# Kernel tuning notes

Measured on AMD Instinct MI355X. Metric: run time of the kernel, lower is better.

Reference implementation:

```python
import jax, jax.numpy as jnp
import numpy as np

B, C, T = 128, 9, 2048
R = T // 4            # reduced_timesteps after two MaxPool1d(2)
N = B * R             # total graph nodes
E_SINGLE = 8192       # edges per sample graph (avg degree 16 over R nodes)
HID = 128
OUT = 12


def setup_inputs():
    key = jax.random.key(0)
    ks = jax.random.split(key, 14)
    x = jax.random.normal(ks[0], (B, C, T), jnp.float32)
    # per-sample graph, replicated with offset i*R per batch element (as in forward)
    single = jax.random.randint(ks[1], (2, E_SINGLE), 0, R)
    offsets = (jnp.arange(B) * R)[None, :, None]
    edge_index = (single[:, None, :] + offsets).reshape(2, -1)  # [2, B*E_SINGLE]

    def lin(k, fan_in, shape):
        return jax.random.normal(k, shape, jnp.float32) / np.sqrt(fan_in)

    return {
        "x": x,
        "edge_index": edge_index,
        "conv1_w": lin(ks[2], C * 5, (16, C, 5)),
        "conv1_b": jnp.zeros((16,), jnp.float32),
        "conv2_w": lin(ks[3], 16 * 5, (32, 16, 5)),
        "conv2_b": jnp.zeros((32,), jnp.float32),
        "gcn1_w": lin(ks[4], 32, (32, HID)),
        "gcn1_b": jnp.zeros((HID,), jnp.float32),
        "gcn2_w": lin(ks[5], HID, (HID, HID)),
        "gcn2_b": jnp.zeros((HID,), jnp.float32),
        "fc_w": lin(ks[6], HID, (HID, OUT)),
        "fc_b": jnp.zeros((OUT,), jnp.float32),
    }


def _gcn_conv(h, edge_index, w, b, n):
    # PyG GCNConv: linear -> add self-loops -> sym-normalized sum aggregation -> + bias
    h = h @ w
    loops = jnp.arange(n)
    row = jnp.concatenate([edge_index[0], loops])  # source
    col = jnp.concatenate([edge_index[1], loops])  # target (aggregation)
    deg = jax.ops.segment_sum(jnp.ones(col.shape, h.dtype), col, num_segments=n)
    dis = jnp.where(deg > 0, jax.lax.rsqrt(jnp.maximum(deg, 1e-12)), 0.0)
    norm = dis[row] * dis[col]                      # [E+N]
    out = jax.ops.segment_sum(norm[:, None] * h[row], col, num_segments=n)
    return out + b


def _temporal_conv(x, w1, b1, w2, b2):
    dn = ("NCH", "OIH", "NCH")
    h = jax.lax.conv_general_dilated(x, w1, (1,), [(2, 2)], dimension_numbers=dn)
    h = jax.nn.relu(h + b1[None, :, None])
    h = jax.lax.reduce_window(h, -jnp.inf, jax.lax.max, (1, 1, 2), (1, 1, 2), "VALID")
    h = jax.lax.conv_general_dilated(h, w2, (1,), [(2, 2)], dimension_numbers=dn)
    h = jax.nn.relu(h + b2[None, :, None])
    h = jax.lax.reduce_window(h, -jnp.inf, jax.lax.max, (1, 1, 2), (1, 1, 2), "VALID")
    return h  # [B, 32, R]


def reference(x, edge_index, conv1_w, conv1_b, conv2_w, conv2_b,
              gcn1_w, gcn1_b, gcn2_w, gcn2_b, fc_w, fc_b):
    h = _temporal_conv(x, conv1_w, conv1_b, conv2_w, conv2_b)   # [B, 32, R]
    nodes = h.transpose(0, 2, 1).reshape(B * R, 32)             # [N, 32]
    g = jax.nn.relu(_gcn_conv(nodes, edge_index, gcn1_w, gcn1_b, N))
    g = jax.nn.relu(_gcn_conv(g, edge_index, gcn2_w, gcn2_b, N))
    g = g.reshape(B, R, HID).mean(axis=1)                       # [B, HID]
    return g @ fc_w + fc_b                                      # [B, OUT]
```

## Files before the change

### kernel.cpp

```cpp
#include <hip/hip_runtime.h>
#include <hip/hip_bf16.h>

#define BB   128
#define CIN  9
#define TT   2048
#define RR   512
#define NN   (BB*RR)
#define HID  128
#define NOUT 12

typedef __attribute__((ext_vector_type(8))) short short8;
typedef __attribute__((ext_vector_type(4))) float f32x4;

static __device__ inline unsigned short f2bf(float f) {
    unsigned int u = __float_as_uint(f);
    unsigned int r = (u + 0x7fffu + ((u >> 16) & 1u)) >> 16;
    return (unsigned short)r;
}
static __device__ inline float bf2f(unsigned short u) {
    return __uint_as_float(((unsigned int)u) << 16);
}

__global__ __launch_bounds__(512) void k_convs(const float* __restrict__ x,
        const float* __restrict__ w1, const float* __restrict__ b1,
        const float* __restrict__ w2, const float* __restrict__ b2,
        unsigned short* __restrict__ nodes16,
        const int* __restrict__ ei, int E, int es,
        int* __restrict__ rptr, float* __restrict__ dis, int* __restrict__ adj,
        const float* __restrict__ g2w, unsigned short* __restrict__ w2t) {
    __shared__ float sx[CIN][268];
    __shared__ float s1[16][132];
    __shared__ int lcnt[512];
    __shared__ int sp[512];
    __shared__ int lcur[512];
    int tid = threadIdx.x;

    if (blockIdx.x == 0) {
        int t = tid;
        lcnt[t] = 0;
        __syncthreads();
        for (int i = t; i < es; i += 512) atomicAdd(&lcnt[ei[E + i]], 1);
        __syncthreads();
        int c = lcnt[t];
        sp[t] = c;
        __syncthreads();
        for (int off = 1; off < 512; off <<= 1) {
            int v = sp[t];
            int add = (t >= off) ? sp[t - off] : 0;
            __syncthreads();
            sp[t] = v + add;
            __syncthreads();
        }
        int excl = sp[t] - c;
        rptr[t] = excl;
        if (t == 511) rptr[512] = es;
        dis[t] = rsqrtf((float)c + 1.0f);
        lcur[t] = excl;
        __syncthreads();
        for (int i = t; i < es; i += 512) {
            int row = ei[i], col = ei[E + i];
            int pos = atomicAdd(&lcur[col], 1);
            adj[pos] = row;
        }
        for (int idx = t; idx < 128 * 128; idx += 512) {
            int c2 = idx >> 7, f = idx & 127;
            w2t[f * 128 + c2] = f2bf(g2w[idx]);
        }
        return;
    }

    int cb = blockIdx.x - 1;
    int b  = cb >> 3;
    int r0 = (cb & 7) * 64;
    int wv   = __builtin_amdgcn_readfirstlane(tid >> 6);
    int lane = tid & 63;

    for (int idx = tid; idx < CIN * 268; idx += 512) {
        int c = idx / 268, j = idx - c * 268;
        int g = 4 * r0 - 6 + j;
        float v = 0.f;
        if (g >= 0 && g < TT) v = x[(b * CIN + c) * TT + g];
        sx[c][j] = v;
    }
    __syncthreads();

    {
        int c1a = wv * 2, c1b = wv * 2 + 1;
        float biasA = b1[c1a], biasB = b1[c1b];
        for (int pp = lane; pp < 132; pp += 64) {
            int p = 2 * r0 - 2 + pp;
            float valA = 0.f, valB = 0.f;
            if (p >= 0 && p < 1024) {
                float a0A = biasA, a1A = biasA, a0B = biasB, a1B = biasB;
#pragma unroll
                for (int c = 0; c < CIN; ++c) {
                    const float2* px = (const float2*)&sx[c][2 * pp];
                    float2 q0 = px[0], q1 = px[1], q2 = px[2];
                    {
                        const float* wp = &w1[(c1a * CIN + c) * 5];
                        float k0 = wp[0], k1 = wp[1], k2 = wp[2], k3 = wp[3], k4 = wp[4];
                        a0A += q0.x*k0 + q0.y*k1 + q1.x*k2 + q1.y*k3 + q2.x*k4;
                        a1A += q0.y*k0 + q1.x*k1 + q1.y*k2 + q2.x*k3 + q2.y*k4;
                    }
                    {
                        const float* wp = &w1[(c1b * CIN + c) * 5];
                        float k0 = wp[0], k1 = wp[1], k2 = wp[2], k3 = wp[3], k4 = wp[4];
                        a0B += q0.x*k0 + q0.y*k1 + q1.x*k2 + q1.y*k3 + q2.x*k4;
                        a1B += q0.y*k0 + q1.x*k1 + q1.y*k2 + q2.x*k3 + q2.y*k4;
                    }
                }
                valA = fmaxf(fmaxf(a0A, a1A), 0.f);
                valB = fmaxf(fmaxf(a0B, a1B), 0.f);
            }
            s1[c1a][pp] = valA;
            s1[c1b][pp] = valB;
        }
    }
    __syncthreads();

    int rl = lane;
    float acc0[4], acc1[4];
#pragma unroll
    for (int o = 0; o < 4; ++o) {
        float bv = b2[wv * 4 + o];
        acc0[o] = bv; acc1[o] = bv;
    }
#pragma unroll
    for (int c = 0; c < 16; ++c) {
        const float2* ps = (const float2*)&s1[c][2 * rl];
        float2 q0 = ps[0], q1 = ps[1], q2 = ps[2];
#pragma unroll
        for (int o = 0; o < 4; ++o) {
            const float* wp = &w2[((wv * 4 + o) * 16 + c) * 5];
            float k0 = wp[0], k1 = wp[1], k2 = wp[2], k3 = wp[3], k4 = wp[4];
            acc0[o] += q0.x*k0 + q0.y*k1 + q1.x*k2 + q1.y*k3 + q2.x*k4;
            acc1[o] += q0.y*k0 + q1.x*k1 + q1.y*k2 + q2.x*k3 + q2.y*k4;
        }
    }
    int n = b * RR + r0 + rl;
    ushort4 ov;
    ov.x = f2bf(fmaxf(fmaxf(acc0[0], acc1[0]), 0.f));
    ov.y = f2bf(fmaxf(fmaxf(acc0[1], acc1[1]), 0.f));
    ov.z = f2bf(fmaxf(fmaxf(acc0[2], acc1[2]), 0.f));
    ov.w = f2bf(fmaxf(fmaxf(acc0[3], acc1[3]), 0.f));
    *(ushort4*)&nodes16[n * 32 + wv * 4] = ov;
}

__global__ __launch_bounds__(256) void k_gl1(const int* __restrict__ rptr,
        const int* __restrict__ adj, const float* __restrict__ dis,
        const unsigned short* __restrict__ nodes16, const float* __restrict__ w,
        const float* __restrict__ bias, unsigned short* __restrict__ h16) {
    __shared__ float srow[32][32];
    __shared__ float sw[32 * 128];
    int bid = (blockIdx.x & 7) * 256 + (blockIdx.x >> 3);
    int tid = threadIdx.x;
    int nbase = bid * 32;
    int b = nbase >> 9;
    const unsigned short* hb = nodes16 + (size_t)b * RR * 32;

    {
        const float4* src = (const float4*)w;
        float4* dst = (float4*)sw;
#pragma unroll
        for (int i = 0; i < 4; ++i) dst[tid + i * 256] = src[tid + i * 256];
    }

    int ln   = tid >> 3;
    int lane = tid & 7;
    int r = (nbase & 511) + ln;
    int s = rptr[r], e = rptr[r + 1];
    float dn = dis[r];
    float4 acc = make_float4(0.f, 0.f, 0.f, 0.f);
    for (int base = s; base < e; base += 8) {
        int j = base + lane;
        int src = 0; float nd = 0.f;
        if (j < e) { src = adj[j]; nd = dis[src]; }
        int cnt = min(8, e - base);
        int k = 0;
        for (; k + 4 <= cnt; k += 4) {
            int   s0 = __shfl(src, k, 8),     s1 = __shfl(src, k + 1, 8);
            int   s2 = __shfl(src, k + 2, 8), s3 = __shfl(src, k + 3, 8);
            float n0 = __shfl(nd, k, 8),      n1 = __shfl(nd, k + 1, 8);
            float n2 = __shfl(nd, k + 2, 8),  n3 = __shfl(nd, k + 3, 8);
            ushort4 u0 = *(const ushort4*)&hb[(size_t)s0 * 32 + lane * 4];
            ushort4 u1 = *(const ushort4*)&hb[(size_t)s1 * 32 + lane * 4];
            ushort4 u2 = *(const ushort4*)&hb[(size_t)s2 * 32 + lane * 4];
            ushort4 u3 = *(const ushort4*)&hb[(size_t)s3 * 32 + lane * 4];
            float w0 = dn * n0, w1 = dn * n1, w2 = dn * n2, w3 = dn * n3;
            acc.x += w0*bf2f(u0.x) + w1*bf2f(u1.x) + w2*bf2f(u2.x) + w3*bf2f(u3.x);
            acc.y += w0*bf2f(u0.y) + w1*bf2f(u1.y) + w2*bf2f(u2.y) + w3*bf2f(u3.y);
            acc.z += w0*bf2f(u0.z) + w1*bf2f(u1.z) + w2*bf2f(u2.z) + w3*bf2f(u3.z);
            acc.w += w0*bf2f(u0.w) + w1*bf2f(u1.w) + w2*bf2f(u2.w) + w3*bf2f(u3.w);
        }
        for (; k < cnt; ++k) {
            int   sk = __shfl(src, k, 8);
            float nk = __shfl(nd, k, 8);
            ushort4 u = *(const ushort4*)&hb[(size_t)sk * 32 + lane * 4];
            float wgt = dn * nk;
            acc.x += wgt * bf2f(u.x); acc.y += wgt * bf2f(u.y);
            acc.z += wgt * bf2f(u.z); acc.w += wgt * bf2f(u.w);
        }
    }
    {
        ushort4 u = *(const ushort4*)&hb[(size_t)r * 32 + lane * 4];
        float wgt = dn * dn;
        acc.x += wgt * bf2f(u.x); acc.y += wgt * bf2f(u.y);
        acc.z += wgt * bf2f(u.z); acc.w += wgt * bf2f(u.w);
    }
    *(float4*)&srow[ln][lane * 4] = acc;
    __syncthreads();

    int fq = tid & 31;
    int ng = tid >> 5;
    float a[4][4];
#pragma unroll
    for (int j = 0; j < 4; ++j)
#pragma unroll
        for (int q = 0; q < 4; ++q) a[j][q] = 0.f;
#pragma unroll
    for (int c = 0; c < 32; ++c) {
        float4 wvv = *(const float4*)&sw[c * 128 + fq * 4];
#pragma unroll
        for (int j = 0; j < 4; ++j) {
            float xc = srow[ng * 4 + j][c];
            a[j][0] += xc * wvv.x; a[j][1] += xc * wvv.y;
            a[j][2] += xc * wvv.z; a[j][3] += xc * wvv.w;
        }
    }
    float4 bv = *(const float4*)&bias[fq * 4];
#pragma unroll
    for (int j = 0; j < 4; ++j) {
        ushort4 o;
        o.x = f2bf(fmaxf(a[j][0] + bv.x, 0.f));
        o.y = f2bf(fmaxf(a[j][1] + bv.y, 0.f));
        o.z = f2bf(fmaxf(a[j][2] + bv.z, 0.f));
        o.w = f2bf(fmaxf(a[j][3] + bv.w, 0.f));
        *(ushort4*)&h16[(size_t)(nbase + ng * 4 + j) * 128 + fq * 4] = o;
    }
}

__global__ __launch_bounds__(256) void k_lin2(const unsigned short* __restrict__ g16,
        const unsigned short* __restrict__ w2t, unsigned short* __restrict__ h16) {
    __shared__ unsigned short srow[64][136];
    __shared__ unsigned short swT[128][136];
    int tid = threadIdx.x;
    int nbase = blockIdx.x * 64;

    {
        const ushort4* src = (const ushort4*)(g16 + (size_t)nbase * 128);
#pragma unroll
        for (int i = 0; i < 8; ++i) {
            int idx = tid + i * 256;
            int row = idx >> 5, col4 = idx & 31;
            ushort4 v = src[idx];
            *(ushort4*)&srow[row][col4 * 4] = v;
        }
    }
    {
        const ushort4* src = (const ushort4*)w2t;
#pragma unroll
        for (int i = 0; i < 16; ++i) {
            int idx = tid + i * 256;
            int f = idx >> 5, c4 = idx & 31;
            ushort4 v = src[idx];
            *(ushort4*)&swT[f][c4 * 4] = v;
        }
    }
    __syncthreads();

    int wv  = tid >> 6;
    int lane = tid & 63;
    int m0 = wv * 16;
    int l15 = lane & 15;
    int quad = lane >> 4;
    f32x4 acc[8];
#pragma unroll
    for (int nt = 0; nt < 8; ++nt) acc[nt] = (f32x4){0.f, 0.f, 0.f, 0.f};
#pragma unroll
    for (int kc = 0; kc < 4; ++kc) {
        int k0 = kc * 32 + quad * 8;
        short8 a = *(const short8*)&srow[m0 + l15][k0];
#pragma unroll
        for (int nt = 0; nt < 8; ++nt) {
            short8 b = *(const short8*)&swT[nt * 16 + l15][k0];
            acc[nt] = __builtin_amdgcn_mfma_f32_16x16x32_bf16(a, b, acc[nt], 0, 0, 0);
        }
    }
#pragma unroll
    for (int nt = 0; nt < 8; ++nt) {
#pragma unroll
        for (int r = 0; r < 4; ++r) {
            int row = m0 + quad * 4 + r;
            int col = nt * 16 + l15;
            h16[(size_t)(nbase + row) * 128 + col] = f2bf(acc[nt][r]);
        }
    }
}

__global__ __launch_bounds__(256) void k_gather128(const int* __restrict__ rptr,
        const int* __restrict__ adj, const float* __restrict__ dis,
        const unsigned short* __restrict__ h, const float* __restrict__ bias,
        float* __restrict__ partial) {
    __shared__ float sred[8][128];
    int bid  = (blockIdx.x & 7) * 1024 + (blockIdx.x >> 3);
    int tid  = threadIdx.x;
    int g    = tid >> 5;
    int lane = tid & 31;
    int node = bid * 8 + g;
    int b = node >> 9;
    int r = node & 511;
    const unsigned short* hb = h + (size_t)b * RR * 128;
    int s = rptr[r], e = rptr[r + 1];
    float dn = dis[r];
    float4 acc = make_float4(0.f, 0.f, 0.f, 0.f);
    for (int base = s; base < e; base += 32) {
        int j = base + lane;
        int src = 0; float nd = 0.f;
        if (j < e) { src = adj[j]; nd = dis[src]; }
        int cnt = min(32, e - base);
        int k = 0;
        for (; k + 4 <= cnt; k += 4) {
            int   s0 = __shfl(src, k, 32),     s1 = __shfl(src, k + 1, 32);
            int   s2 = __shfl(src, k + 2, 32), s3 = __shfl(src, k + 3, 32);
            float n0 = __shfl(nd, k, 32),      n1 = __shfl(nd, k + 1, 32);
            float n2 = __shfl(nd, k + 2, 32),  n3 = __shfl(nd, k + 3, 32);
            ushort4 u0 = *(const ushort4*)&hb[(size_t)s0 * 128 + lane * 4];
            ushort4 u1 = *(const ushort4*)&hb[(size_t)s1 * 128 + lane * 4];
            ushort4 u2 = *(const ushort4*)&hb[(size_t)s2 * 128 + lane * 4];
            ushort4 u3 = *(const ushort4*)&hb[(size_t)s3 * 128 + lane * 4];
            float w0 = dn * n0, w1 = dn * n1, w2 = dn * n2, w3 = dn * n3;
            acc.x += w0*bf2f(u0.x) + w1*bf2f(u1.x) + w2*bf2f(u2.x) + w3*bf2f(u3.x);
            acc.y += w0*bf2f(u0.y) + w1*bf2f(u1.y) + w2*bf2f(u2.y) + w3*bf2f(u3.y);
            acc.z += w0*bf2f(u0.z) + w1*bf2f(u1.z) + w2*bf2f(u2.z) + w3*bf2f(u3.z);
            acc.w += w0*bf2f(u0.w) + w1*bf2f(u1.w) + w2*bf2f(u2.w) + w3*bf2f(u3.w);
        }
        for (; k < cnt; ++k) {
            int   sk = __shfl(src, k, 32);
            float nk = __shfl(nd, k, 32);
            ushort4 u = *(const ushort4*)&hb[(size_t)sk * 128 + lane * 4];
            float wgt = dn * nk;
            acc.x += wgt * bf2f(u.x); acc.y += wgt * bf2f(u.y);
            acc.z += wgt * bf2f(u.z); acc.w += wgt * bf2f(u.w);
        }
    }
    ushort4 u = *(const ushort4*)&hb[(size_t)r * 128 + lane * 4];
    float wgt = dn * dn;
    float4 bv = *(const float4*)&bias[lane * 4];
    acc.x = fmaxf(acc.x + wgt * bf2f(u.x) + bv.x, 0.f);
    acc.y = fmaxf(acc.y + wgt * bf2f(u.y) + bv.y, 0.f);
    acc.z = fmaxf(acc.z + wgt * bf2f(u.z) + bv.z, 0.f);
    acc.w = fmaxf(acc.w + wgt * bf2f(u.w) + bv.w, 0.f);
    *(float4*)&sred[g][lane * 4] = acc;
    __syncthreads();
    if (tid < 128) {
        float ssum = 0.f;
#pragma unroll
        for (int j = 0; j < 8; ++j) ssum += sred[j][tid];
        partial[(size_t)bid * 128 + tid] = ssum;
    }
}

__global__ __launch_bounds__(128) void k_fc(const float* __restrict__ partial,
        const float* __restrict__ fw, const float* __restrict__ fb,
        float* __restrict__ out) {
    __shared__ float sm[HID];
    int b = blockIdx.x, f = threadIdx.x;
    float acc = 0.f;
#pragma unroll 8
    for (int j = 0; j < 64; ++j) acc += partial[(size_t)(b * 64 + j) * 128 + f];
    sm[f] = acc * (1.0f / RR);
    __syncthreads();
    if (f < NOUT) {
        float s = fb[f];
#pragma unroll
        for (int c = 0; c < HID; ++c) s += sm[c] * fw[c * NOUT + f];
        out[b * NOUT + f] = s;
    }
}

extern "C" void kernel_launch(void* const* d_in, const int* in_sizes, int n_in,
                              void* d_out, int out_size, void* d_ws, size_t ws_size,
                              hipStream_t stream) {
    const float* x   = (const float*)d_in[0];
    const int*   ei  = (const int*)d_in[1];
    const float* c1w = (const float*)d_in[2];
    const float* c1b = (const float*)d_in[3];
    const float* c2w = (const float*)d_in[4];
    const float* c2b = (const float*)d_in[5];
    const float* g1w = (const float*)d_in[6];
    const float* g1b = (const float*)d_in[7];
    const float* g2w = (const float*)d_in[8];
    const float* g2b = (const float*)d_in[9];
    const float* fw  = (const float*)d_in[10];
    const float* fb  = (const float*)d_in[11];
    float* out = (float*)d_out;
    int E  = in_sizes[1] / 2;
    int es = E / BB;

    char* ws = (char*)d_ws;
    unsigned short* nodes16 = (unsigned short*)(ws);
    unsigned short* bufA16  = (unsigned short*)(ws + (4u << 20));
    unsigned short* bufC16  = (unsigned short*)(ws + (20u << 20));
    int*   rptr    = (int*)  (ws + (36u << 20));
    float* dis     = (float*)(ws + (36u << 20) + 4096);
    int*   adj     = (int*)  (ws + (36u << 20) + 8192);
    unsigned short* w2t = (unsigned short*)(ws + (36u << 20) + 65536);
    float* partial = (float*)(ws + (37u << 20));

    k_convs<<<BB * 8 + 1, 512, 0, stream>>>(x, c1w, c1b, c2w, c2b, nodes16,
                                            ei, E, es, rptr, dis, adj, g2w, w2t);

    k_gl1<<<NN / 32, 256, 0, stream>>>(rptr, adj, dis, nodes16, g1w, g1b, bufA16);

    k_lin2<<<NN / 64, 256, 0, stream>>>(bufA16, w2t, bufC16);
    k_gather128<<<NN / 8, 256, 0, stream>>>(rptr, adj, dis, bufC16, g2b, partial);

    k_fc<<<BB, 128, 0, stream>>>(partial, fw, fb, out);
}
```

Before: 171.8 us.

## Replace sparse GCN gathers with dense normalized-adjacency MFMA matmuls

Since every sample shares one 512-node graph, the code builds a dense 512x512 normalized adjacency once: degree counts, then scattered atomic adds of the norm weights plus self-loops, converted to bf16. The CSR build and the per-node irregular gathers are removed. Both GCN aggregations become bf16 MFMA GEMMs over feature matrices stored node-transposed. The second aggregation also fuses bias, ReLU and the node mean reduction, so the final FC reduces far fewer partials. This swaps irregular memory access for dense compute, adds two small launches, and rounds the adjacency weights to bf16.

```diff
diff --git a/kernel.cpp b/kernel.cpp
--- a/kernel.cpp
+++ b/kernel.cpp
@@ -21,55 +21,65 @@
     return __uint_as_float(((unsigned int)u) << 16);
 }
 
+__global__ __launch_bounds__(256) void k_prep(const int* __restrict__ ei, int E, int es,
+        float* __restrict__ Af32, float* __restrict__ dis,
+        const float* __restrict__ g2w, unsigned short* __restrict__ w2t) {
+    int tid = threadIdx.x;
+    if (blockIdx.x == 0) {
+        __shared__ int cnt[512];
+        cnt[tid] = 0; cnt[tid + 256] = 0;
+        __syncthreads();
+        for (int i = tid; i < es; i += 256) atomicAdd(&cnt[ei[E + i]], 1);
+        __syncthreads();
+        dis[tid]       = rsqrtf((float)cnt[tid] + 1.0f);
+        dis[tid + 256] = rsqrtf((float)cnt[tid + 256] + 1.0f);
+        for (int idx = tid; idx < 128 * 128; idx += 256) {
+            int c2 = idx >> 7, f = idx & 127;
+            w2t[f * 128 + c2] = f2bf(g2w[idx]);
+        }
+    } else {
+        float4* dst = (float4*)(Af32 + (size_t)(blockIdx.x - 1) * 2048);
+        float4 z = make_float4(0.f, 0.f, 0.f, 0.f);
+        dst[tid] = z;
+        dst[tid + 256] = z;
+    }
+}
+
+__global__ __launch_bounds__(256) void k_scatter(const int* __restrict__ ei, int E, int es,
+        const float* __restrict__ dis, float* __restrict__ Af32) {
+    int i = blockIdx.x * 256 + threadIdx.x;
+    if (i < es) {
+        int row = ei[i], col = ei[E + i];
+        atomicAdd(&Af32[col * 512 + row], dis[row] * dis[col]);
+    } else if (i < es + 512) {
+        int r = i - es;
+        float d = dis[r];
+        atomicAdd(&Af32[r * 512 + r], d * d);
+    }
+}
+
 __global__ __launch_bounds__(512) void k_convs(const float* __restrict__ x,
         const float* __restrict__ w1, const float* __restrict__ b1,
         const float* __restrict__ w2, const float* __restrict__ b2,
-        unsigned short* __restrict__ nodes16,
-        const int* __restrict__ ei, int E, int es,
-        int* __restrict__ rptr, float* __restrict__ dis, int* __restrict__ adj,
-        const float* __restrict__ g2w, unsigned short* __restrict__ w2t) {
+        unsigned short* __restrict__ nodesT,
+        const float* __restrict__ Af32, unsigned short* __restrict__ Ab16) {
     __shared__ float sx[CIN][268];
     __shared__ float s1[16][132];
-    __shared__ int lcnt[512];
-    __shared__ int sp[512];
-    __shared__ int lcur[512];
     int tid = threadIdx.x;
 
-    if (blockIdx.x == 0) {
-        int t = tid;
-        lcnt[t] = 0;
-        __syncthreads();
-        for (int i = t; i < es; i += 512) atomicAdd(&lcnt[ei[E + i]], 1);
-        __syncthreads();
-        int c = lcnt[t];
-        sp[t] = c;
-        __syncthreads();
-        for (int off = 1; off < 512; off <<= 1) {
-            int v = sp[t];
-            int add = (t >= off) ? sp[t - off] : 0;
-            __syncthreads();
-            sp[t] = v + add;
-            __syncthreads();
-        }
-        int excl = sp[t] - c;
-        rptr[t] = excl;
-        if (t == 511) rptr[512] = es;
-        dis[t] = rsqrtf((float)c + 1.0f);
-        lcur[t] = excl;
-        __syncthreads();
-        for (int i = t; i < es; i += 512) {
-            int row = ei[i], col = ei[E + i];
-            int pos = atomicAdd(&lcur[col], 1);
-            adj[pos] = row;
-        }
-        for (int idx = t; idx < 128 * 128; idx += 512) {
-            int c2 = idx >> 7, f = idx & 127;
-            w2t[f * 128 + c2] = f2bf(g2w[idx]);
-        }
+    if (blockIdx.x >= 1024) {
+        int idx0 = (((blockIdx.x - 1024) << 9) + tid) << 3;
+        float4 v0 = *(const float4*)&Af32[idx0];
+        float4 v1 = *(const float4*)&Af32[idx0 + 4];
+        ushort4 o0, o1;
+        o0.x = f2bf(v0.x); o0.y = f2bf(v0.y); o0.z = f2bf(v0.z); o0.w = f2bf(v0.w);
+        o1.x = f2bf(v1.x); o1.y = f2bf(v1.y); o1.z = f2bf(v1.z); o1.w = f2bf(v1.w);
+        *(ushort4*)&Ab16[idx0] = o0;
+        *(ushort4*)&Ab16[idx0 + 4] = o1;
         return;
     }
 
-    int cb = blockIdx.x - 1;
+    int cb = blockIdx.x;
     int b  = cb >> 3;
     int r0 = (cb & 7) * 64;
     int wv   = __builtin_amdgcn_readfirstlane(tid >> 6);
@@ -137,112 +147,119 @@
             acc1[o] += q0.y*k0 + q1.x*k1 + q1.y*k2 + q2.x*k3 + q2.y*k4;
         }
     }
-    int n = b * RR + r0 + rl;
-    ushort4 ov;
-    ov.x = f2bf(fmaxf(fmaxf(acc0[0], acc1[0]), 0.f));
-    ov.y = f2bf(fmaxf(fmaxf(acc0[1], acc1[1]), 0.f));
-    ov.z = f2bf(fmaxf(fmaxf(acc0[2], acc1[2]), 0.f));
-    ov.w = f2bf(fmaxf(fmaxf(acc0[3], acc1[3]), 0.f));
-    *(ushort4*)&nodes16[n * 32 + wv * 4] = ov;
-}
-
-__global__ __launch_bounds__(256) void k_gl1(const int* __restrict__ rptr,
-        const int* __restrict__ adj, const float* __restrict__ dis,
-        const unsigned short* __restrict__ nodes16, const float* __restrict__ w,
-        const float* __restrict__ bias, unsigned short* __restrict__ h16) {
-    __shared__ float srow[32][32];
-    __shared__ float sw[32 * 128];
-    int bid = (blockIdx.x & 7) * 256 + (blockIdx.x >> 3);
+    int n = r0 + rl;
+    unsigned short* np = nodesT + ((size_t)b * 32 + wv * 4) * 512 + n;
+    np[0]    = f2bf(fmaxf(fmaxf(acc0[0], acc1[0]), 0.f));
+    np[512]  = f2bf(fmaxf(fmaxf(acc0[1], acc1[1]), 0.f));
+    np[1024] = f2bf(fmaxf(fmaxf(acc0[2], acc1[2]), 0.f));
+    np[1536] = f2bf(fmaxf(fmaxf(acc0[3], acc1[3]), 0.f));
+}
+
+__global__ __launch_bounds__(256) void k_agg1(const unsigned short* __restrict__ Ab,
+        const unsigned short* __restrict__ nT, const float* __restrict__ w1,
+        const float* __restrict__ b1, unsigned short* __restrict__ h16) {
+    __shared__ unsigned short sA[128][72];
+    __shared__ unsigned short sN[32][72];
+    __shared__ float sAgg[128][33];
+    __shared__ float sw1[32 * 128];
     int tid = threadIdx.x;
-    int nbase = bid * 32;
-    int b = nbase >> 9;
-    const unsigned short* hb = nodes16 + (size_t)b * RR * 32;
+    int b  = blockIdx.x >> 2;
+    int rb = blockIdx.x & 3;
+    int r0 = rb * 128;
+    const unsigned short* nb = nT + (size_t)b * 32 * 512;
 
     {
-        const float4* src = (const float4*)w;
-        float4* dst = (float4*)sw;
+        const float4* src = (const float4*)w1;
+        float4* dst = (float4*)sw1;
 #pragma unroll
         for (int i = 0; i < 4; ++i) dst[tid + i * 256] = src[tid + i * 256];
     }
 
-    int ln   = tid >> 3;
-    int lane = tid & 7;
-    int r = (nbase & 511) + ln;
-    int s = rptr[r], e = rptr[r + 1];
-    float dn = dis[r];
-    float4 acc = make_float4(0.f, 0.f, 0.f, 0.f);
-    for (int base = s; base < e; base += 8) {
-        int j = base + lane;
-        int src = 0; float nd = 0.f;
-        if (j < e) { src = adj[j]; nd = dis[src]; }
-        int cnt = min(8, e - base);
-        int k = 0;
-        for (; k + 4 <= cnt; k += 4) {
-            int   s0 = __shfl(src, k, 8),     s1 = __shfl(src, k + 1, 8);
-            int   s2 = __shfl(src, k + 2, 8), s3 = __shfl(src, k + 3, 8);
-            float n0 = __shfl(nd, k, 8),      n1 = __shfl(nd, k + 1, 8);
-            float n2 = __shfl(nd, k + 2, 8),  n3 = __shfl(nd, k + 3, 8);
-            ushort4 u0 = *(const ushort4*)&hb[(size_t)s0 * 32 + lane * 4];
-            ushort4 u1 = *(const ushort4*)&hb[(size_t)s1 * 32 + lane * 4];
-            ushort4 u2 = *(const ushort4*)&hb[(size_t)s2 * 32 + lane * 4];
-            ushort4 u3 = *(const ushort4*)&hb[(size_t)s3 * 32 + lane * 4];
-            float w0 = dn * n0, w1 = dn * n1, w2 = dn * n2, w3 = dn * n3;
-            acc.x += w0*bf2f(u0.x) + w1*bf2f(u1.x) + w2*bf2f(u2.x) + w3*bf2f(u3.x);
-            acc.y += w0*bf2f(u0.y) + w1*bf2f(u1.y) + w2*bf2f(u2.y) + w3*bf2f(u3.y);
-            acc.z += w0*bf2f(u0.z) + w1*bf2f(u1.z) + w2*bf2f(u2.z) + w3*bf2f(u3.z);
-            acc.w += w0*bf2f(u0.w) + w1*bf2f(u1.w) + w2*bf2f(u2.w) + w3*bf2f(u3.w);
-        }
-        for (; k < cnt; ++k) {
-            int   sk = __shfl(src, k, 8);
-            float nk = __shfl(nd, k, 8);
-            ushort4 u = *(const ushort4*)&hb[(size_t)sk * 32 + lane * 4];
-            float wgt = dn * nk;
-            acc.x += wgt * bf2f(u.x); acc.y += wgt * bf2f(u.y);
-            acc.z += wgt * bf2f(u.z); acc.w += wgt * bf2f(u.w);
-        }
-    }
-    {
-        ushort4 u = *(const ushort4*)&hb[(size_t)r * 32 + lane * 4];
-        float wgt = dn * dn;
-        acc.x += wgt * bf2f(u.x); acc.y += wgt * bf2f(u.y);
-        acc.z += wgt * bf2f(u.z); acc.w += wgt * bf2f(u.w);
-    }
-    *(float4*)&srow[ln][lane * 4] = acc;
+    int wv = tid >> 6, lane = tid & 63;
+    int l15 = lane & 15, quad = lane >> 4;
+    int mB = wv * 32;
+    f32x4 acc[2][2];
+#pragma unroll
+    for (int i = 0; i < 2; ++i)
+#pragma unroll
+        for (int j = 0; j < 2; ++j) acc[i][j] = (f32x4){0.f, 0.f, 0.f, 0.f};
+
+    for (int kt = 0; kt < 8; ++kt) {
+        int k0 = kt * 64;
+        __syncthreads();
+#pragma unroll
+        for (int i = 0; i < 8; ++i) {
+            int idx = tid + i * 256;
+            int row = idx >> 4, c4 = (idx & 15) * 4;
+            *(ushort4*)&sA[row][c4] = *(const ushort4*)&Ab[(size_t)(r0 + row) * 512 + k0 + c4];
+        }
+#pragma unroll
+        for (int i = 0; i < 2; ++i) {
+            int idx = tid + i * 256;
+            int f = idx >> 4, c4 = (idx & 15) * 4;
+            *(ushort4*)&sN[f][c4] = *(const ushort4*)&nb[(size_t)f * 512 + k0 + c4];
+        }
+        __syncthreads();
+#pragma unroll
+        for (int ks = 0; ks < 2; ++ks) {
+            int kk = ks * 32 + quad * 8;
+            short8 av0 = *(const short8*)&sA[mB + l15][kk];
+            short8 av1 = *(const short8*)&sA[mB + 16 + l15][kk];
+            short8 bv0 = *(const short8*)&sN[l15][kk];
+            short8 bv1 = *(const short8*)&sN[16 + l15][kk];
+            acc[0][0] = __builtin_amdgcn_mfma_f32_16x16x32_bf16(av0, bv0, acc[0][0], 0, 0, 0);
+            acc[0][1] = __builtin_amdgcn_mfma_f32_16x16x32_bf16(av0, bv1, acc[0][1], 0, 0, 0);
+            acc[1][0] = __builtin_amdgcn_mfma_f32_16x16x32_bf16(av1, bv0, acc[1][0], 0, 0, 0);
+            acc[1][1] = __builtin_amdgcn_mfma_f32_16x16x32_bf16(av1, bv1, acc[1][1], 0, 0, 0);
+        }
+    }
+    __syncthreads();
+#pragma unroll
+    for (int mi = 0; mi < 2; ++mi)
+#pragma unroll
+        for (int ni = 0; ni < 2; ++ni)
+#pragma unroll
+            for (int r = 0; r < 4; ++r)
+                sAgg[mB + mi * 16 + quad * 4 + r][ni * 16 + l15] = acc[mi][ni][r];
     __syncthreads();
 
     int fq = tid & 31;
     int ng = tid >> 5;
-    float a[4][4];
-#pragma unroll
-    for (int j = 0; j < 4; ++j)
-#pragma unroll
-        for (int q = 0; q < 4; ++q) a[j][q] = 0.f;
-#pragma unroll
-    for (int c = 0; c < 32; ++c) {
-        float4 wvv = *(const float4*)&sw[c * 128 + fq * 4];
+    float4 bv = *(const float4*)&b1[fq * 4];
+    for (int ch = 0; ch < 4; ++ch) {
+        float a[4][4];
+#pragma unroll
+        for (int j = 0; j < 4; ++j)
+#pragma unroll
+            for (int q = 0; q < 4; ++q) a[j][q] = 0.f;
+#pragma unroll
+        for (int c = 0; c < 32; ++c) {
+            float4 wvv = *(const float4*)&sw1[c * 128 + fq * 4];
+#pragma unroll
+            for (int j = 0; j < 4; ++j) {
+                float xc = sAgg[ch * 32 + ng * 4 + j][c];
+                a[j][0] += xc * wvv.x; a[j][1] += xc * wvv.y;
+                a[j][2] += xc * wvv.z; a[j][3] += xc * wvv.w;
+            }
+        }
 #pragma unroll
         for (int j = 0; j < 4; ++j) {
-            float xc = srow[ng * 4 + j][c];
-            a[j][0] += xc * wvv.x; a[j][1] += xc * wvv.y;
-            a[j][2] += xc * wvv.z; a[j][3] += xc * wvv.w;
-        }
-    }
-    float4 bv = *(const float4*)&bias[fq * 4];
-#pragma unroll
-    for (int j = 0; j < 4; ++j) {
-        ushort4 o;
-        o.x = f2bf(fmaxf(a[j][0] + bv.x, 0.f));
-        o.y = f2bf(fmaxf(a[j][1] + bv.y, 0.f));
-        o.z = f2bf(fmaxf(a[j][2] + bv.z, 0.f));
-        o.w = f2bf(fmaxf(a[j][3] + bv.w, 0.f));
-        *(ushort4*)&h16[(size_t)(nbase + ng * 4 + j) * 128 + fq * 4] = o;
+            ushort4 o;
+            o.x = f2bf(fmaxf(a[j][0] + bv.x, 0.f));
+            o.y = f2bf(fmaxf(a[j][1] + bv.y, 0.f));
+            o.z = f2bf(fmaxf(a[j][2] + bv.z, 0.f));
+            o.w = f2bf(fmaxf(a[j][3] + bv.w, 0.f));
+            *(ushort4*)&h16[(size_t)(b * 512 + r0 + ch * 32 + ng * 4 + j) * 128 + fq * 4] = o;
+        }
     }
 }
 
 __global__ __launch_bounds__(256) void k_lin2(const unsigned short* __restrict__ g16,
-        const unsigned short* __restrict__ w2t, unsigned short* __restrict__ h16) {
-    __shared__ unsigned short srow[64][136];
-    __shared__ unsigned short swT[128][136];
+        const unsigned short* __restrict__ w2t, unsigned short* __restrict__ tT) {
+    __shared__ __align__(16) unsigned short smem2[64 * 136 + 128 * 136];
+    unsigned short (*srow)[136] = (unsigned short (*)[136])smem2;
+    unsigned short (*swT)[136]  = (unsigned short (*)[136])&smem2[64 * 136];
+    unsigned short (*sOut)[72]  = (unsigned short (*)[72])smem2;
     int tid = threadIdx.x;
     int nbase = blockIdx.x * 64;
 
@@ -286,78 +303,99 @@
             acc[nt] = __builtin_amdgcn_mfma_f32_16x16x32_bf16(a, b, acc[nt], 0, 0, 0);
         }
     }
+    __syncthreads();
+
 #pragma unroll
     for (int nt = 0; nt < 8; ++nt) {
-#pragma unroll
-        for (int r = 0; r < 4; ++r) {
-            int row = m0 + quad * 4 + r;
-            int col = nt * 16 + l15;
-            h16[(size_t)(nbase + row) * 128 + col] = f2bf(acc[nt][r]);
-        }
-    }
-}
-
-__global__ __launch_bounds__(256) void k_gather128(const int* __restrict__ rptr,
-        const int* __restrict__ adj, const float* __restrict__ dis,
-        const unsigned short* __restrict__ h, const float* __restrict__ bias,
+        ushort4 o;
+        o.x = f2bf(acc[nt][0]); o.y = f2bf(acc[nt][1]);
+        o.z = f2bf(acc[nt][2]); o.w = f2bf(acc[nt][3]);
+        *(ushort4*)&sOut[nt * 16 + l15][m0 + quad * 4] = o;
+    }
+    __syncthreads();
+
+    int b = nbase >> 9;
+    int rl0 = nbase & 511;
+#pragma unroll
+    for (int i = 0; i < 8; ++i) {
+        int idx = tid + i * 256;
+        int col = idx >> 4, r4 = (idx & 15) * 4;
+        ushort4 v = *(ushort4*)&sOut[col][r4];
+        *(ushort4*)&tT[((size_t)(b * 128 + col)) * 512 + rl0 + r4] = v;
+    }
+}
+
+__global__ __launch_bounds__(256) void k_agg2(const unsigned short* __restrict__ Ab,
+        const unsigned short* __restrict__ tT, const float* __restrict__ b2,
         float* __restrict__ partial) {
-    __shared__ float sred[8][128];
-    int bid  = (blockIdx.x & 7) * 1024 + (blockIdx.x >> 3);
-    int tid  = threadIdx.x;
-    int g    = tid >> 5;
-    int lane = tid & 31;
-    int node = bid * 8 + g;
-    int b = node >> 9;
-    int r = node & 511;
-    const unsigned short* hb = h + (size_t)b * RR * 128;
-    int s = rptr[r], e = rptr[r + 1];
-    float dn = dis[r];
-    float4 acc = make_float4(0.f, 0.f, 0.f, 0.f);
-    for (int base = s; base < e; base += 32) {
-        int j = base + lane;
-        int src = 0; float nd = 0.f;
-        if (j < e) { src = adj[j]; nd = dis[src]; }
-        int cnt = min(32, e - base);
-        int k = 0;
-        for (; k + 4 <= cnt; k += 4) {
-            int   s0 = __shfl(src, k, 32),     s1 = __shfl(src, k + 1, 32);
-            int   s2 = __shfl(src, k + 2, 32), s3 = __shfl(src, k + 3, 32);
-            float n0 = __shfl(nd, k, 32),      n1 = __shfl(nd, k + 1, 32);
-            float n2 = __shfl(nd, k + 2, 32),  n3 = __shfl(nd, k + 3, 32);
-            ushort4 u0 = *(const ushort4*)&hb[(size_t)s0 * 128 + lane * 4];
-            ushort4 u1 = *(const ushort4*)&hb[(size_t)s1 * 128 + lane * 4];
-            ushort4 u2 = *(const ushort4*)&hb[(size_t)s2 * 128 + lane * 4];
-            ushort4 u3 = *(const ushort4*)&hb[(size_t)s3 * 128 + lane * 4];
-            float w0 = dn * n0, w1 = dn * n1, w2 = dn * n2, w3 = dn * n3;
-            acc.x += w0*bf2f(u0.x) + w1*bf2f(u1.x) + w2*bf2f(u2.x) + w3*bf2f(u3.x);
-            acc.y += w0*bf2f(u0.y) + w1*bf2f(u1.y) + w2*bf2f(u2.y) + w3*bf2f(u3.y);
-            acc.z += w0*bf2f(u0.z) + w1*bf2f(u1.z) + w2*bf2f(u2.z) + w3*bf2f(u3.z);
-            acc.w += w0*bf2f(u0.w) + w1*bf2f(u1.w) + w2*bf2f(u2.w) + w3*bf2f(u3.w);
-        }
-        for (; k < cnt; ++k) {
-            int   sk = __shfl(src, k, 32);
-            float nk = __shfl(nd, k, 32);
-            ushort4 u = *(const ushort4*)&hb[(size_t)sk * 128 + lane * 4];
-            float wgt = dn * nk;
-            acc.x += wgt * bf2f(u.x); acc.y += wgt * bf2f(u.y);
-            acc.z += wgt * bf2f(u.z); acc.w += wgt * bf2f(u.w);
-        }
-    }
-    ushort4 u = *(const ushort4*)&hb[(size_t)r * 128 + lane * 4];
-    float wgt = dn * dn;
-    float4 bv = *(const float4*)&bias[lane * 4];
-    acc.x = fmaxf(acc.x + wgt * bf2f(u.x) + bv.x, 0.f);
-    acc.y = fmaxf(acc.y + wgt * bf2f(u.y) + bv.y, 0.f);
-    acc.z = fmaxf(acc.z + wgt * bf2f(u.z) + bv.z, 0.f);
-    acc.w = fmaxf(acc.w + wgt * bf2f(u.w) + bv.w, 0.f);
-    *(float4*)&sred[g][lane * 4] = acc;
-    __syncthreads();
-    if (tid < 128) {
-        float ssum = 0.f;
-#pragma unroll
-        for (int j = 0; j < 8; ++j) ssum += sred[j][tid];
-        partial[(size_t)bid * 128 + tid] = ssum;
-    }
+    __shared__ unsigned short sA[128][72];
+    __shared__ unsigned short sB[128][72];
+    __shared__ float sred[2][128];
+    int tid = threadIdx.x;
+    int b  = blockIdx.x >> 2;
+    int rb = blockIdx.x & 3;
+    int r0 = rb * 128;
+    const unsigned short* tb = tT + (size_t)b * 128 * 512;
+    int wv = tid >> 6, lane = tid & 63;
+    int l15 = lane & 15, quad = lane >> 4;
+    int wr = wv >> 1, wc = wv & 1;
+    f32x4 acc[4][4];
+#pragma unroll
+    for (int i = 0; i < 4; ++i)
+#pragma unroll
+        for (int j = 0; j < 4; ++j) acc[i][j] = (f32x4){0.f, 0.f, 0.f, 0.f};
+
+    for (int kt = 0; kt < 8; ++kt) {
+        int k0 = kt * 64;
+        __syncthreads();
+#pragma unroll
+        for (int i = 0; i < 8; ++i) {
+            int idx = tid + i * 256;
+            int row = idx >> 4, c4 = (idx & 15) * 4;
+            *(ushort4*)&sA[row][c4] = *(const ushort4*)&Ab[(size_t)(r0 + row) * 512 + k0 + c4];
+        }
+#pragma unroll
+        for (int i = 0; i < 8; ++i) {
+            int idx = tid + i * 256;
+            int row = idx >> 4, c4 = (idx & 15) * 4;
+            *(ushort4*)&sB[row][c4] = *(const ushort4*)&tb[(size_t)row * 512 + k0 + c4];
+        }
+        __syncthreads();
+#pragma unroll
+        for (int ks = 0; ks < 2; ++ks) {
+            int kk = ks * 32 + quad * 8;
+            short8 av[4], bfr[4];
+#pragma unroll
+            for (int mi = 0; mi < 4; ++mi)
+                av[mi] = *(const short8*)&sA[wr * 64 + mi * 16 + l15][kk];
+#pragma unroll
+            for (int ni = 0; ni < 4; ++ni)
+                bfr[ni] = *(const short8*)&sB[wc * 64 + ni * 16 + l15][kk];
+#pragma unroll
+            for (int mi = 0; mi < 4; ++mi)
+#pragma unroll
+                for (int ni = 0; ni < 4; ++ni)
+                    acc[mi][ni] = __builtin_amdgcn_mfma_f32_16x16x32_bf16(av[mi], bfr[ni], acc[mi][ni], 0, 0, 0);
+        }
+    }
+
+#pragma unroll
+    for (int ni = 0; ni < 4; ++ni) {
+        int col = wc * 64 + ni * 16 + l15;
+        float bc = b2[col];
+        float s = 0.f;
+#pragma unroll
+        for (int mi = 0; mi < 4; ++mi)
+#pragma unroll
+            for (int r = 0; r < 4; ++r)
+                s += fmaxf(acc[mi][ni][r] + bc, 0.f);
+        s += __shfl_xor(s, 16);
+        s += __shfl_xor(s, 32);
+        if (quad == 0) sred[wr][col] = s;
+    }
+    __syncthreads();
+    if (tid < 128)
+        partial[(size_t)blockIdx.x * 128 + tid] = sred[0][tid] + sred[1][tid];
 }
 
 __global__ __launch_bounds__(128) void k_fc(const float* __restrict__ partial,
@@ -366,8 +404,8 @@
     __shared__ float sm[HID];
     int b = blockIdx.x, f = threadIdx.x;
     float acc = 0.f;
-#pragma unroll 8
-    for (int j = 0; j < 64; ++j) acc += partial[(size_t)(b * 64 + j) * 128 + f];
+#pragma unroll
+    for (int j = 0; j < 4; ++j) acc += partial[(size_t)(b * 4 + j) * 128 + f];
     sm[f] = acc * (1.0f / RR);
     __syncthreads();
     if (f < NOUT) {
@@ -398,22 +436,24 @@
     int es = E / BB;
 
     char* ws = (char*)d_ws;
-    unsigned short* nodes16 = (unsigned short*)(ws);
-    unsigned short* bufA16  = (unsigned short*)(ws + (4u << 20));
-    unsigned short* bufC16  = (unsigned short*)(ws + (20u << 20));
-    int*   rptr    = (int*)  (ws + (36u << 20));
-    float* dis     = (float*)(ws + (36u << 20) + 4096);
-    int*   adj     = (int*)  (ws + (36u << 20) + 8192);
-    unsigned short* w2t = (unsigned short*)(ws + (36u << 20) + 65536);
-    float* partial = (float*)(ws + (37u << 20));
-
-    k_convs<<<BB * 8 + 1, 512, 0, stream>>>(x, c1w, c1b, c2w, c2b, nodes16,
-                                            ei, E, es, rptr, dis, adj, g2w, w2t);
-
-    k_gl1<<<NN / 32, 256, 0, stream>>>(rptr, adj, dis, nodes16, g1w, g1b, bufA16);
-
-    k_lin2<<<NN / 64, 256, 0, stream>>>(bufA16, w2t, bufC16);
-    k_gather128<<<NN / 8, 256, 0, stream>>>(rptr, adj, dis, bufC16, g2b, partial);
+    unsigned short* nodesT = (unsigned short*)(ws);
+    unsigned short* h1     = (unsigned short*)(ws + (4u << 20));
+    unsigned short* tT     = (unsigned short*)(ws + (20u << 20));
+    float* Af32            = (float*)(ws + (36u << 20));
+    unsigned short* Ab16   = (unsigned short*)(ws + (37u << 20));
+    float* partial         = (float*)(ws + (37u << 20) + (512u << 10));
+    float* dis             = (float*)(ws + (37u << 20) + (768u << 10));
+    unsigned short* w2t    = (unsigned short*)(ws + (37u << 20) + (772u << 10));
+
+    k_prep<<<129, 256, 0, stream>>>(ei, E, es, Af32, dis, g2w, w2t);
+    k_scatter<<<(es + 512 + 255) / 256, 256, 0, stream>>>(ei, E, es, dis, Af32);
+
+    k_convs<<<1024 + 64, 512, 0, stream>>>(x, c1w, c1b, c2w, c2b, nodesT, Af32, Ab16);
+
+    k_agg1<<<512, 256, 0, stream>>>(Ab16, nodesT, g1w, g1b, h1);
+
+    k_lin2<<<NN / 64, 256, 0, stream>>>(h1, w2t, tT);
+    k_agg2<<<512, 256, 0, stream>>>(Ab16, tT, g2b, partial);
 
     k_fc<<<BB, 128, 0, stream>>>(partial, fw, fb, out);
 }
```

New measurement: 187.9 us. +9.4%, slower.
